# Kernel tuning notes

Hardware: AMD Instinct MI355X
Metric: run time of the kernel (lower is better)

## Reference

```python
import jax, jax.numpy as jnp
import numpy as np

T = 2_097_152  # timesteps


def setup_inputs() -> dict:
    key = jax.random.key(0)
    # precipitation P and potential evapotranspiration E, in mm/day
    x = jax.random.uniform(key, (T, 2), dtype=jnp.float32) * 10.0
    x1 = jnp.float32(350.0)  # production store capacity (mm)
    return {"x": x, "x1": x1}


def reference(x, x1):
    # GR4J production storage. s_init = 0.0.
    P = x[:, 0]
    E = x[:, 1]
    p_n = jax.nn.relu(P - E)  # net rainfall
    e_n = jax.nn.relu(E - P)  # net evapotranspiration
    # tanh(p_n/x1), tanh(e_n/x1) only depend on inputs -> precompute (same math)
    t_p = jnp.tanh(p_n / x1)
    t_e = jnp.tanh(e_n / x1)
    s0 = jnp.float32(0.0) * x1  # s_init * x1

    def step(s, te):
        tp, tn = te
        r = s / x1
        p_s = x1 * (1.0 - r ** 2) * tp / (1.0 + r * tp)
        e_s = s * (2.0 - r) * tn / (1.0 + (1.0 - r) * tn)
        s = s + p_s - e_s
        perc = s * (1.0 - (1.0 + ((4.0 / 9.0) * s / x1) ** 4) ** (-0.25))
        s = s - perc
        return s, (p_s, perc, s)

    _, (p_s, perc, s_store) = jax.lax.scan(step, s0, (t_p, t_e))

    # concat([p_n[:,None], e_n[:,None], p_s[:,None], perc[:,None]], axis=1)
    out = jnp.stack([p_n, e_n, p_s, perc], axis=1)  # [T, 4]
    # scale=True with mu/sigma None: standardize with batch statistics
    mu = jnp.mean(out, axis=0)
    sigma = jnp.std(out, axis=0)  # population std, matches tf.math.reduce_std
    out = (out - mu) / sigma
    return out, s_store[:, None]
```

## Files before the change

kernel.cpp:

```cpp
#include <hip/hip_runtime.h>


typedef float f32x4 __attribute__((ext_vector_type(4)));

#define LCH      32
#define CPB      128
#define TPB      256
#define BSTEPS   4096
#define WUP      1536
#define WUMAP    96
#define WSTO     12
#define NMAP     352
#define HODD     176
#define NCK      129
#define NMST     4

#define CC1 0.98078528f
#define CC2 0.92387953f
#define CC3 0.83146961f
#define CC4 0.70710678f
#define CC5 0.55557023f
#define CC6 0.38268343f
#define CC7 0.19509032f

__device__ __forceinline__ void stepk(float& s, const f32x4 k, float gma) {
    float s2m = s * s;
    float t1  = fmaf(k.y, s, k.x);
    float t2  = fmaf(k.w, s, k.z);
    float s1  = fmaf(s2m, t2, t1);
    float w2  = s1 * s1;
    float q4  = gma * s1;
    float w4  = w2 * w2;
    s = fmaf(-q4, w4, s1);
}

__device__ __forceinline__ void stepk_m(float& s, const f32x4 k, float gma,
                                        float& ps_o, float& pc_o) {
    float sp  = s;
    float s2m = s * s;
    float t1  = fmaf(k.y, s, k.x);
    float t2  = fmaf(k.w, s, k.z);
    float s1  = fmaf(s2m, t2, t1);
    float w2  = s1 * s1;
    float q4  = gma * s1;
    float w4  = w2 * w2;
    s = fmaf(-q4, w4, s1);
    ps_o = fmaxf(s1 - sp, 0.0f);
    pc_o = q4 * w4;
}

struct KC { float inv, x1, x1sq, x1_2, two_x1cu, five_x1sq, four_x1; };

__device__ __forceinline__ f32x4 mkk(float P, float Ev, const KC c,
                                     float& pn_o, float& en_o) {
    float d  = P - Ev;
    float pn = fmaxf(d, 0.f), en = fmaxf(-d, 0.f);
    float up = pn * c.inv, un = en * c.inv;
    float tp = up * fmaf(up * up, -(1.f/3.f), 1.f);
    float tn = un * fmaf(un * un, -(1.f/3.f), 1.f);
    float al = tp * c.inv, be = tn * c.inv;
    float a2 = al * al,  a3v = a2 * al;
    float b2 = be * be,  b3v = b2 * be;
    float e2 = fmaf(-be, c.x1, 1.f);
    float k0 = tp * c.x1;
    float k1 = 1.f - a2 * c.x1sq - (c.x1_2 * be * e2 + c.two_x1cu * b3v);
    float k2 = (a3v * c.x1sq - al) - (c.x1_2 * b2 - be * e2 - c.five_x1sq * b3v);
    float k3 = a2 + b2 - c.four_x1 * b3v;
    pn_o = pn; en_o = en;
    return (f32x4){k0, k1, k2, k3};
}

__global__ __launch_bounds__(256, 2) void scan_hexa(
        const float* __restrict__ x, const float* __restrict__ x1p,
        f32x4* __restrict__ pspc4, f32x4* __restrict__ s4,
        float* __restrict__ partials) {
    __shared__ f32x4 tk[32 * NCK];
    __shared__ f32x4 mapA[NMAP];
    __shared__ f32x4 mapB[NMAP];
    __shared__ float red[32];

    const int tid  = threadIdx.x;
    const int lane = tid & 63;
    const int wid  = tid >> 6;
    const int b    = blockIdx.x;

    const float x1 = x1p[0];
    KC c;
    c.inv = 1.0f / x1; c.x1 = x1; c.x1sq = x1 * x1; c.x1_2 = 2.0f * x1;
    c.two_x1cu = 2.0f * x1 * c.x1sq; c.five_x1sq = 5.0f * c.x1sq;
    c.four_x1 = 4.0f * x1;
    const float gma = 64.0f / (6561.0f * c.x1sq * c.x1sq);
    const float cen = (184.0f / 350.0f) * x1;
    const float hw  = (208.0f / 350.0f) * x1;
    const float ihw = 1.0f / hw;

    float snode[8];
    {
        const float ND[8] = { CC1,  CC3,  CC5,  CC7, -CC7, -CC5, -CC3, -CC1};
        #pragma unroll
        for (int j = 0; j < 8; ++j) snode[j] = fmaf(hw, ND[j], cen);
    }

    float spn = 0.f, sen = 0.f, qpn = 0.f, qen = 0.f;

    {
        const f32x4* __restrict__ x4 = (const f32x4*)x;
        const f32x4 z4 = (f32x4){0.f, 0.f, 0.f, 0.f};

        auto build = [&](const int mi, f32x4 (&w)[8]) {
            const int m = mi - WUMAP;
            float sv[8];
            #pragma unroll
            for (int j = 0; j < 8; ++j) sv[j] = snode[j];
            const bool mainm = (m >= 0);
            #pragma unroll
            for (int q = 0; q < 8; ++q) {
                float pn0, en0, pn1, en1;
                const f32x4 kA = mkk(w[q].x, w[q].y, c, pn0, en0);
                const f32x4 kB = mkk(w[q].z, w[q].w, c, pn1, en1);
                #pragma unroll
                for (int j = 0; j < 8; ++j) {
                    stepk(sv[j], kA, gma);
                    stepk(sv[j], kB, gma);
                }
                if (mainm) {
                    spn += pn0 + pn1; sen += en0 + en1;
                    qpn = fmaf(pn0, pn0, fmaf(pn1, pn1, qpn));
                    qen = fmaf(en0, en0, fmaf(en1, en1, qen));
                    const int t = 16 * m + 2 * q;
                    const int r = t & 31, col = t >> 5;
                    tk[r * NCK + col]       = kA;
                    tk[(r + 1) * NCK + col] = kB;
                }
            }
            float v[8];
            #pragma unroll
            for (int j = 0; j < 8; ++j) v[j] = (sv[j] - cen) * ihw;
            const float e0 = v[0] + v[7], e1 = v[1] + v[6];
            const float e2 = v[2] + v[5], e3 = v[3] + v[4];
            const float o0 = v[0] - v[7], o1 = v[1] - v[6];
            const float o2 = v[2] - v[5], o3 = v[3] - v[4];
            const float a0 = 0.125f * (e0 + e1 + e2 + e3);
            const float a1 = 0.25f * (o0*CC1 + o1*CC3 + o2*CC5 + o3*CC7);
            const float a2 = 0.25f * ((e0 - e3)*CC2 + (e1 - e2)*CC6);
            const float a3 = 0.25f * (o0*CC3 - o1*CC7 - o2*CC1 - o3*CC5);
            const float a4 = 0.25f * CC4 * ((e0 + e3) - (e1 + e2));
            const float a5 = 0.25f * (o0*CC5 - o1*CC1 + o2*CC7 + o3*CC3);
            const float a6 = 0.25f * ((e0 - e3)*CC6 - (e1 - e2)*CC2);
            const float a7 = 0.25f * (o0*CC7 - o1*CC5 + o2*CC3 - o3*CC1);
            const f32x4 ra = (f32x4){a0 - a2 + a4 - a6,
                                     a1 - 3.0f*a3 + 5.0f*a5 - 7.0f*a7,
                                     2.0f*a2 - 8.0f*a4 + 18.0f*a6,
                                     4.0f*a3 - 20.0f*a5 + 56.0f*a7};
            const f32x4 rb = (f32x4){8.0f*a4 - 48.0f*a6,
                                     16.0f*a5 - 112.0f*a7,
                                     32.0f*a6,
                                     64.0f*a7};
            const int slot = (mi >> 1) + ((mi & 1) ? HODD : 0);
            mapA[slot] = ra;
            mapB[slot] = rb;
        };

        const long base = (long)b * (BSTEPS / 2);
        f32x4 wa[8], wb[8];
        const long gpA = base + 8L * (tid - WUMAP);
        #pragma unroll
        for (int q = 0; q < 8; ++q) {
            const long g = gpA + q;
            wa[q] = (g >= 0) ? x4[g] : z4;
        }
        const bool hasB = (tid < NMAP - 256);
        const long gpB = base + 8L * (tid + 256 - WUMAP);
        #pragma unroll
        for (int q = 0; q < 8; ++q)
            wb[q] = hasB ? x4[gpB + q] : z4;
        build(tid, wa);
        if (hasB) build(tid + 256, wb);
    }
    __syncthreads();

    float aps = 0.f, apc = 0.f, qps = 0.f, qpc = 0.f;
    float sg = 0.f;
    if (tid < CPB) {
        const int l = tid;
        const long gstart = ((long)b * CPB + l) * LCH;
        const float s0 = (gstart >= WUP) ? 0.47f * x1 : 0.0f;
        sg = (s0 - cen) * ihw;
        f32x4 PA[8], PB[8], QA[8], QB[8];
        auto rdw = [&](f32x4 (&A)[8], f32x4 (&B)[8], const int st) {
            const int base = l + 4 * st;
            #pragma unroll
            for (int u = 0; u < 8; ++u)
                A[u] = mapA[base + (u >> 1) + ((u & 1) ? HODD : 0)];
            #pragma unroll
            for (int u = 0; u < 8; ++u)
                B[u] = mapB[base + (u >> 1) + ((u & 1) ? HODD : 0)];
        };
        auto wstp = [&](f32x4 (&A)[8], f32x4 (&B)[8]) {
            #pragma unroll
            for (int u = 0; u < 8; ++u) {
                const float s2  = sg * sg;
                const float p0  = fmaf(A[u].y, sg, A[u].x);
                const float p1  = fmaf(A[u].w, sg, A[u].z);
                const float p2  = fmaf(B[u].y, sg, B[u].x);
                const float p3  = fmaf(B[u].w, sg, B[u].z);
                const float s4v = s2 * s2;
                const float q0  = fmaf(p1, s2, p0);
                const float q1  = fmaf(p3, s2, p2);
                sg = fmaf(q1, s4v, q0);
            }
        };
        rdw(PA, PB, 0);
        #pragma unroll 1
        for (int st = 0; st < WSTO; st += 2) {
            rdw(QA, QB, st + 1);
            wstp(PA, PB);
            rdw(PA, PB, st + 2 < WSTO ? st + 2 : WSTO - 1);
            wstp(QA, QB);
        }
    }
    const float s_after = fmaf(hw, sg, cen);

    if (tid < CPB) {
        const int l = tid;
        const size_t chunk = (size_t)b * CPB + l;
        float s = s_after;
        f32x4 KP[8], KQ[8];
        auto rdk = [&](f32x4 (&K)[8], const int m) {
            const int base = (m << 3) * NCK + l;
            #pragma unroll
            for (int u = 0; u < 8; ++u) K[u] = tk[base + u * NCK];
        };
        auto mst = [&](f32x4 (&K)[8], const int m) {
            float psv[8], pcv[8], sv[8];
            #pragma unroll
            for (int u = 0; u < 8; ++u) {
                stepk_m(s, K[u], gma, psv[u], pcv[u]);
                sv[u] = s;
            }
            #pragma unroll
            for (int u = 0; u < 8; ++u) {
                aps += psv[u]; apc += pcv[u];
                qps = fmaf(psv[u], psv[u], qps); qpc = fmaf(pcv[u], pcv[u], qpc);
            }
            const size_t pb = chunk * 16 + 4 * m;
            pspc4[pb + 0] = (f32x4){psv[0], pcv[0], psv[1], pcv[1]};
            pspc4[pb + 1] = (f32x4){psv[2], pcv[2], psv[3], pcv[3]};
            pspc4[pb + 2] = (f32x4){psv[4], pcv[4], psv[5], pcv[5]};
            pspc4[pb + 3] = (f32x4){psv[6], pcv[6], psv[7], pcv[7]};
            const size_t sb = chunk * 8 + 2 * m;
            s4[sb]     = (f32x4){sv[0], sv[1], sv[2], sv[3]};
            s4[sb + 1] = (f32x4){sv[4], sv[5], sv[6], sv[7]};
        };
        rdk(KP, 0);
        #pragma unroll 1
        for (int m = 0; m < NMST; m += 2) {
            rdk(KQ, m + 1);
            mst(KP, m);
            rdk(KP, m + 2 < NMST ? m + 2 : NMST - 1);
            mst(KQ, m + 1);
        }
    }

    float vals[8] = {spn, sen, aps, apc, qpn, qen, qps, qpc};
    #pragma unroll
    for (int k = 0; k < 8; ++k) {
        float v = vals[k];
        #pragma unroll
        for (int off = 32; off > 0; off >>= 1) v += __shfl_down(v, off, 64);
        if (lane == 0) red[k * 4 + wid] = v;
    }
    __syncthreads();
    if (tid < 8)
        partials[b * 8 + tid] =
            red[tid * 4] + red[tid * 4 + 1] + red[tid * 4 + 2] + red[tid * 4 + 3];
}

__global__ __launch_bounds__(256) void normalize_stats(
        const float* __restrict__ x, const f32x4* __restrict__ pspc4,
        const float* __restrict__ pA, f32x4* __restrict__ out4,
        int nA, int Thalf, int T) {
    __shared__ float red[256];
    __shared__ float sst[8];
    const int tid = threadIdx.x;
    {
        const int c = tid & 7;
        float v = 0.f;
        for (int i = tid >> 3; i < nA; i += 32) v += pA[i * 8 + c];
        red[tid] = v;
        __syncthreads();
        for (int off = 128; off >= 8; off >>= 1) {
            if (tid < off) red[tid] += red[tid + off];
            __syncthreads();
        }
        if (tid == 0) {
            const float invT = 1.0f / (float)T;
            #pragma unroll
            for (int k = 0; k < 4; ++k) {
                float mu  = red[k] * invT;
                float var = fmaxf(fmaf(-mu, mu, red[4 + k] * invT), 0.0f);
                sst[k]     = mu;
                sst[4 + k] = (var > 0.0f) ? rsqrtf(var) : 0.0f;
            }
        }
        __syncthreads();
    }
    const float mu0 = sst[0], mu1 = sst[1], mu2 = sst[2], mu3 = sst[3];
    const float is0 = sst[4], is1 = sst[5], is2 = sst[6], is3 = sst[7];
    const f32x4* __restrict__ x4 = (const f32x4*)x;
    for (int i = blockIdx.x * 256 + tid; i < Thalf; i += 1024 * 256) {
        f32x4 xv = x4[i];
        f32x4 pq = pspc4[i];
        float d0 = xv.x - xv.y, d1 = xv.z - xv.w;
        out4[2 * i]     = (f32x4){(fmaxf(d0, 0.f) - mu0) * is0,
                                  (fmaxf(-d0, 0.f) - mu1) * is1,
                                  (pq.x - mu2) * is2,
                                  (pq.y - mu3) * is3};
        out4[2 * i + 1] = (f32x4){(fmaxf(d1, 0.f) - mu0) * is0,
                                  (fmaxf(-d1, 0.f) - mu1) * is1,
                                  (pq.z - mu2) * is2,
                                  (pq.w - mu3) * is3};
    }
}

#define L_CHUNK  128
#define FB_WARMUP 2048
__device__ __forceinline__ float inv1p_fb(float a) {
    float i1 = 1.0f - a;
    float i2 = fmaf(-a, i1, 1.0f);
    return fmaf(-a, i2, 1.0f);
}
struct SCfb { float x1, inv_x1, c49; };
__device__ __forceinline__ void scan_step_fb(float& s, float P, float E, const SCfb c,
                                             float& pn, float& en, float& ps, float& pc) {
    float d = P - E;
    float pn_ = fmaxf(d, 0.0f), en_ = fmaxf(-d, 0.0f);
    float up = pn_ * c.inv_x1;
    float tp = up * fmaf(up * up, -(1.0f / 3.0f), 1.0f);
    float un = en_ * c.inv_x1;
    float tn = un * fmaf(un * un, -(1.0f / 3.0f), 1.0f);
    float r = s * c.inv_x1;
    float ps_ = (tp * c.x1) * fmaf(-r, r, 1.0f) * inv1p_fb(r * tp);
    float es_ = (s * (2.0f - r)) * tn * inv1p_fb((1.0f - r) * tn);
    float s1 = s + ps_ - es_;
    float z = s1 * c.c49, z2 = z * z, v = z2 * z2;
    float t = fmaf(v, fmaf(v, 0.15625f, -0.25f), 1.0f);
    float s2 = s1 * t;
    pn = pn_; en = en_; ps = ps_; pc = s1 - s2; s = s2;
}
__global__ __launch_bounds__(256) void scan_kernel_fb(
        const float* __restrict__ x, const float* __restrict__ x1ptr,
        float* __restrict__ out, float* __restrict__ s_store,
        float* __restrict__ partials, int T) {
    const int c = blockIdx.x * blockDim.x + threadIdx.x;
    const int nchunks = (T + L_CHUNK - 1) / L_CHUNK;
    SCfb cc; cc.x1 = x1ptr[0]; cc.inv_x1 = 1.0f / cc.x1; cc.c49 = (4.0f / 9.0f) * cc.inv_x1;
    float s1a[4] = {0.f, 0.f, 0.f, 0.f};
    float s2a[4] = {0.f, 0.f, 0.f, 0.f};
    if (c < nchunks) {
        const int g0 = c * L_CHUNK;
        const int g1 = min(g0 + L_CHUNK, T);
        const int w0 = max(g0 - FB_WARMUP, 0);
        float s = 0.0f; float pn, en, ps, pc;
        const float2* __restrict__ x2 = (const float2*)x;
        for (int t = w0; t < g0; ++t) { float2 xv = x2[t]; scan_step_fb(s, xv.x, xv.y, cc, pn, en, ps, pc); }
        float4* __restrict__ out4 = (float4*)out;
        for (int t = g0; t < g1; ++t) {
            float2 xv = x2[t];
            scan_step_fb(s, xv.x, xv.y, cc, pn, en, ps, pc);
            out4[t] = make_float4(pn, en, ps, pc);
            s_store[t] = s;
            s1a[0] += pn; s1a[1] += en; s1a[2] += ps; s1a[3] += pc;
            s2a[0] = fmaf(pn, pn, s2a[0]); s2a[1] = fmaf(en, en, s2a[1]);
            s2a[2] = fmaf(ps, ps, s2a[2]); s2a[3] = fmaf(pc, pc, s2a[3]);
        }
    }
    __shared__ float red[256];
    float vals[8] = {s1a[0], s1a[1], s1a[2], s1a[3], s2a[0], s2a[1], s2a[2], s2a[3]};
    for (int k = 0; k < 8; ++k) {
        red[threadIdx.x] = vals[k];
        __syncthreads();
        for (int off = 128; off > 0; off >>= 1) {
            if ((int)threadIdx.x < off) red[threadIdx.x] += red[threadIdx.x + off];
            __syncthreads();
        }
        if (threadIdx.x == 0) partials[blockIdx.x * 8 + k] = red[0];
        __syncthreads();
    }
}
__global__ __launch_bounds__(64) void finalize_fb(
        const float* __restrict__ partials, float* __restrict__ stats, int nblk, int T) {
    const int lane = threadIdx.x;
    float v[8] = {0.f, 0.f, 0.f, 0.f, 0.f, 0.f, 0.f, 0.f};
    for (int b = lane; b < nblk; b += 64)
        for (int k = 0; k < 8; ++k) v[k] += partials[b * 8 + k];
    #pragma unroll
    for (int k = 0; k < 8; ++k)
        for (int off = 32; off > 0; off >>= 1) v[k] += __shfl_down(v[k], off, 64);
    if (lane == 0) {
        const float invT = 1.0f / (float)T;
        for (int k = 0; k < 4; ++k) {
            float mu = v[k] * invT;
            float var = fmaxf(fmaf(-mu, mu, v[k + 4] * invT), 0.0f);
            stats[k] = mu;
            stats[4 + k] = (var > 0.0f) ? rsqrtf(var) : 0.0f;
        }
    }
}
__global__ __launch_bounds__(256) void normalize_fb(
        float* __restrict__ out, const float* __restrict__ stats, int T) {
    const int t = blockIdx.x * blockDim.x + threadIdx.x;
    if (t >= T) return;
    const float4 mu = *(const float4*)stats;
    const float4 is = *(const float4*)(stats + 4);
    float4* o4 = (float4*)out;
    float4 v = o4[t];
    v.x = (v.x - mu.x) * is.x; v.y = (v.y - mu.y) * is.y;
    v.z = (v.z - mu.z) * is.z; v.w = (v.w - mu.w) * is.w;
    o4[t] = v;
}

extern "C" void kernel_launch(void* const* d_in, const int* in_sizes, int n_in,
                              void* d_out, int out_size, void* d_ws, size_t ws_size,
                              hipStream_t stream) {
    const float* x  = (const float*)d_in[0];
    const float* x1 = (const float*)d_in[1];
    const int T = in_sizes[0] / 2;

    float* out     = (float*)d_out;
    float* s_store = out + 4 * (size_t)T;

    const int nblk = T / BSTEPS;

    float* pA = (float*)d_ws;
    const size_t pq_off = 4608;
    const size_t need = (pq_off + 2 * (size_t)T) * sizeof(float);

    const bool fast = (T % BSTEPS == 0) && nblk >= 1 && nblk <= 512 &&
                      (ws_size >= need);

    if (fast) {
        f32x4* pspc4 = (f32x4*)((float*)d_ws + pq_off);
        scan_hexa<<<nblk, TPB, 0, stream>>>(x, x1, pspc4, (f32x4*)s_store, pA);
        normalize_stats<<<1024, 256, 0, stream>>>(x, pspc4, pA,
                                                  (f32x4*)out, nblk, T / 2, T);
    } else {
        float* stats    = (float*)d_ws;
        float* partials = stats + 8;
        const int nchunks = (T + L_CHUNK - 1) / L_CHUNK;
        const int nblkA = (nchunks + 255) / 256;
        scan_kernel_fb<<<nblkA, 256, 0, stream>>>(x, x1, out, s_store, partials, T);
        finalize_fb<<<1, 64, 0, stream>>>(partials, stats, nblkA, T);
        normalize_fb<<<(T + 255) / 256, 256, 0, stream>>>(out, stats, T);
    }
}
```

Measured before the change: 111.1 us.

## Use 384-thread blocks so each thread builds one map, drop software prefetch

Raises the scan block size from 256 to 384 threads so each of the 352 map-building entries gets its own thread, instead of 96 threads doing a second serial build. The launch bound moves to 3 blocks per CU and the block reduction now covers six waves. The double-buffered register prefetch in the warmup and main scan loops is replaced by simple single-buffer loops, which lowers register pressure to fit the new occupancy target but exposes LDS read latency in the serial chains.

```diff
diff --git a/kernel.cpp b/kernel.cpp
--- a/kernel.cpp
+++ b/kernel.cpp
@@ -5,7 +5,7 @@
 
 #define LCH      32
 #define CPB      128
-#define TPB      256
+#define TPB      384
 #define BSTEPS   4096
 #define WUP      1536
 #define WUMAP    96
@@ -14,6 +14,7 @@
 #define HODD     176
 #define NCK      129
 #define NMST     4
+#define NWAVE    6
 
 #define CC1 0.98078528f
 #define CC2 0.92387953f
@@ -70,14 +71,14 @@
     return (f32x4){k0, k1, k2, k3};
 }
 
-__global__ __launch_bounds__(256, 2) void scan_hexa(
+__global__ __launch_bounds__(TPB, 3) void scan_h384(
         const float* __restrict__ x, const float* __restrict__ x1p,
         f32x4* __restrict__ pspc4, f32x4* __restrict__ s4,
         float* __restrict__ partials) {
     __shared__ f32x4 tk[32 * NCK];
     __shared__ f32x4 mapA[NMAP];
     __shared__ f32x4 mapB[NMAP];
-    __shared__ float red[32];
+    __shared__ float red[8 * NWAVE];
 
     const int tid  = threadIdx.x;
     const int lane = tid & 63;
@@ -94,88 +95,75 @@
     const float hw  = (208.0f / 350.0f) * x1;
     const float ihw = 1.0f / hw;
 
-    float snode[8];
-    {
-        const float ND[8] = { CC1,  CC3,  CC5,  CC7, -CC7, -CC5, -CC3, -CC1};
-        #pragma unroll
-        for (int j = 0; j < 8; ++j) snode[j] = fmaf(hw, ND[j], cen);
-    }
-
     float spn = 0.f, sen = 0.f, qpn = 0.f, qen = 0.f;
 
-    {
+    if (tid < NMAP) {
         const f32x4* __restrict__ x4 = (const f32x4*)x;
         const f32x4 z4 = (f32x4){0.f, 0.f, 0.f, 0.f};
-
-        auto build = [&](const int mi, f32x4 (&w)[8]) {
-            const int m = mi - WUMAP;
-            float sv[8];
-            #pragma unroll
-            for (int j = 0; j < 8; ++j) sv[j] = snode[j];
-            const bool mainm = (m >= 0);
-            #pragma unroll
-            for (int q = 0; q < 8; ++q) {
-                float pn0, en0, pn1, en1;
-                const f32x4 kA = mkk(w[q].x, w[q].y, c, pn0, en0);
-                const f32x4 kB = mkk(w[q].z, w[q].w, c, pn1, en1);
-                #pragma unroll
-                for (int j = 0; j < 8; ++j) {
-                    stepk(sv[j], kA, gma);
-                    stepk(sv[j], kB, gma);
-                }
-                if (mainm) {
-                    spn += pn0 + pn1; sen += en0 + en1;
-                    qpn = fmaf(pn0, pn0, fmaf(pn1, pn1, qpn));
-                    qen = fmaf(en0, en0, fmaf(en1, en1, qen));
-                    const int t = 16 * m + 2 * q;
-                    const int r = t & 31, col = t >> 5;
-                    tk[r * NCK + col]       = kA;
-                    tk[(r + 1) * NCK + col] = kB;
-                }
-            }
-            float v[8];
-            #pragma unroll
-            for (int j = 0; j < 8; ++j) v[j] = (sv[j] - cen) * ihw;
-            const float e0 = v[0] + v[7], e1 = v[1] + v[6];
-            const float e2 = v[2] + v[5], e3 = v[3] + v[4];
-            const float o0 = v[0] - v[7], o1 = v[1] - v[6];
-            const float o2 = v[2] - v[5], o3 = v[3] - v[4];
-            const float a0 = 0.125f * (e0 + e1 + e2 + e3);
-            const float a1 = 0.25f * (o0*CC1 + o1*CC3 + o2*CC5 + o3*CC7);
-            const float a2 = 0.25f * ((e0 - e3)*CC2 + (e1 - e2)*CC6);
-            const float a3 = 0.25f * (o0*CC3 - o1*CC7 - o2*CC1 - o3*CC5);
-            const float a4 = 0.25f * CC4 * ((e0 + e3) - (e1 + e2));
-            const float a5 = 0.25f * (o0*CC5 - o1*CC1 + o2*CC7 + o3*CC3);
-            const float a6 = 0.25f * ((e0 - e3)*CC6 - (e1 - e2)*CC2);
-            const float a7 = 0.25f * (o0*CC7 - o1*CC5 + o2*CC3 - o3*CC1);
-            const f32x4 ra = (f32x4){a0 - a2 + a4 - a6,
-                                     a1 - 3.0f*a3 + 5.0f*a5 - 7.0f*a7,
-                                     2.0f*a2 - 8.0f*a4 + 18.0f*a6,
-                                     4.0f*a3 - 20.0f*a5 + 56.0f*a7};
-            const f32x4 rb = (f32x4){8.0f*a4 - 48.0f*a6,
-                                     16.0f*a5 - 112.0f*a7,
-                                     32.0f*a6,
-                                     64.0f*a7};
-            const int slot = (mi >> 1) + ((mi & 1) ? HODD : 0);
-            mapA[slot] = ra;
-            mapB[slot] = rb;
-        };
-
-        const long base = (long)b * (BSTEPS / 2);
-        f32x4 wa[8], wb[8];
-        const long gpA = base + 8L * (tid - WUMAP);
+        const long gp = (long)b * (BSTEPS / 2) + 8L * (tid - WUMAP);
+        f32x4 w[8];
         #pragma unroll
         for (int q = 0; q < 8; ++q) {
-            const long g = gpA + q;
-            wa[q] = (g >= 0) ? x4[g] : z4;
-        }
-        const bool hasB = (tid < NMAP - 256);
-        const long gpB = base + 8L * (tid + 256 - WUMAP);
-        #pragma unroll
-        for (int q = 0; q < 8; ++q)
-            wb[q] = hasB ? x4[gpB + q] : z4;
-        build(tid, wa);
-        if (hasB) build(tid + 256, wb);
+            const long g = gp + q;
+            w[q] = (g >= 0) ? x4[g] : z4;
+        }
+
+        float snode[8];
+        {
+            const float ND[8] = { CC1,  CC3,  CC5,  CC7, -CC7, -CC5, -CC3, -CC1};
+            #pragma unroll
+            for (int j = 0; j < 8; ++j) snode[j] = fmaf(hw, ND[j], cen);
+        }
+
+        const int m = tid - WUMAP;
+        const bool mainm = (m >= 0);
+        float sv[8];
+        #pragma unroll
+        for (int j = 0; j < 8; ++j) sv[j] = snode[j];
+        #pragma unroll
+        for (int q = 0; q < 8; ++q) {
+            float pn0, en0, pn1, en1;
+            const f32x4 kA = mkk(w[q].x, w[q].y, c, pn0, en0);
+            const f32x4 kB = mkk(w[q].z, w[q].w, c, pn1, en1);
+            #pragma unroll
+            for (int j = 0; j < 8; ++j) {
+                stepk(sv[j], kA, gma);
+                stepk(sv[j], kB, gma);
+            }
+            if (mainm) {
+                spn += pn0 + pn1; sen += en0 + en1;
+                qpn = fmaf(pn0, pn0, fmaf(pn1, pn1, qpn));
+                qen = fmaf(en0, en0, fmaf(en1, en1, qen));
+                const int t = 16 * m + 2 * q;
+                const int r = t & 31, col = t >> 5;
+                tk[r * NCK + col]       = kA;
+                tk[(r + 1) * NCK + col] = kB;
+            }
+        }
+        float v[8];
+        #pragma unroll
+        for (int j = 0; j < 8; ++j) v[j] = (sv[j] - cen) * ihw;
+        const float e0 = v[0] + v[7], e1 = v[1] + v[6];
+        const float e2 = v[2] + v[5], e3 = v[3] + v[4];
+        const float o0 = v[0] - v[7], o1 = v[1] - v[6];
+        const float o2 = v[2] - v[5], o3 = v[3] - v[4];
+        const float a0 = 0.125f * (e0 + e1 + e2 + e3);
+        const float a1 = 0.25f * (o0*CC1 + o1*CC3 + o2*CC5 + o3*CC7);
+        const float a2 = 0.25f * ((e0 - e3)*CC2 + (e1 - e2)*CC6);
+        const float a3 = 0.25f * (o0*CC3 - o1*CC7 - o2*CC1 - o3*CC5);
+        const float a4 = 0.25f * CC4 * ((e0 + e3) - (e1 + e2));
+        const float a5 = 0.25f * (o0*CC5 - o1*CC1 + o2*CC7 + o3*CC3);
+        const float a6 = 0.25f * ((e0 - e3)*CC6 - (e1 - e2)*CC2);
+        const float a7 = 0.25f * (o0*CC7 - o1*CC5 + o2*CC3 - o3*CC1);
+        const int slot = (tid >> 1) + ((tid & 1) ? HODD : 0);
+        mapA[slot] = (f32x4){a0 - a2 + a4 - a6,
+                             a1 - 3.0f*a3 + 5.0f*a5 - 7.0f*a7,
+                             2.0f*a2 - 8.0f*a4 + 18.0f*a6,
+                             4.0f*a3 - 20.0f*a5 + 56.0f*a7};
+        mapB[slot] = (f32x4){8.0f*a4 - 48.0f*a6,
+                             16.0f*a5 - 112.0f*a7,
+                             32.0f*a6,
+                             64.0f*a7};
     }
     __syncthreads();
 
@@ -186,8 +174,9 @@
         const long gstart = ((long)b * CPB + l) * LCH;
         const float s0 = (gstart >= WUP) ? 0.47f * x1 : 0.0f;
         sg = (s0 - cen) * ihw;
-        f32x4 PA[8], PB[8], QA[8], QB[8];
-        auto rdw = [&](f32x4 (&A)[8], f32x4 (&B)[8], const int st) {
+        f32x4 A[8], B[8];
+        #pragma unroll 1
+        for (int st = 0; st < WSTO; ++st) {
             const int base = l + 4 * st;
             #pragma unroll
             for (int u = 0; u < 8; ++u)
@@ -195,8 +184,6 @@
             #pragma unroll
             for (int u = 0; u < 8; ++u)
                 B[u] = mapB[base + (u >> 1) + ((u & 1) ? HODD : 0)];
-        };
-        auto wstp = [&](f32x4 (&A)[8], f32x4 (&B)[8]) {
             #pragma unroll
             for (int u = 0; u < 8; ++u) {
                 const float s2  = sg * sg;
@@ -209,14 +196,6 @@
                 const float q1  = fmaf(p3, s2, p2);
                 sg = fmaf(q1, s4v, q0);
             }
-        };
-        rdw(PA, PB, 0);
-        #pragma unroll 1
-        for (int st = 0; st < WSTO; st += 2) {
-            rdw(QA, QB, st + 1);
-            wstp(PA, PB);
-            rdw(PA, PB, st + 2 < WSTO ? st + 2 : WSTO - 1);
-            wstp(QA, QB);
         }
     }
     const float s_after = fmaf(hw, sg, cen);
@@ -225,13 +204,12 @@
         const int l = tid;
         const size_t chunk = (size_t)b * CPB + l;
         float s = s_after;
-        f32x4 KP[8], KQ[8];
-        auto rdk = [&](f32x4 (&K)[8], const int m) {
+        f32x4 K[8];
+        #pragma unroll 1
+        for (int m = 0; m < NMST; ++m) {
             const int base = (m << 3) * NCK + l;
             #pragma unroll
             for (int u = 0; u < 8; ++u) K[u] = tk[base + u * NCK];
-        };
-        auto mst = [&](f32x4 (&K)[8], const int m) {
             float psv[8], pcv[8], sv[8];
             #pragma unroll
             for (int u = 0; u < 8; ++u) {
@@ -251,14 +229,6 @@
             const size_t sb = chunk * 8 + 2 * m;
             s4[sb]     = (f32x4){sv[0], sv[1], sv[2], sv[3]};
             s4[sb + 1] = (f32x4){sv[4], sv[5], sv[6], sv[7]};
-        };
-        rdk(KP, 0);
-        #pragma unroll 1
-        for (int m = 0; m < NMST; m += 2) {
-            rdk(KQ, m + 1);
-            mst(KP, m);
-            rdk(KP, m + 2 < NMST ? m + 2 : NMST - 1);
-            mst(KQ, m + 1);
         }
     }
 
@@ -268,12 +238,15 @@
         float v = vals[k];
         #pragma unroll
         for (int off = 32; off > 0; off >>= 1) v += __shfl_down(v, off, 64);
-        if (lane == 0) red[k * 4 + wid] = v;
+        if (lane == 0) red[k * NWAVE + wid] = v;
     }
     __syncthreads();
-    if (tid < 8)
-        partials[b * 8 + tid] =
-            red[tid * 4] + red[tid * 4 + 1] + red[tid * 4 + 2] + red[tid * 4 + 3];
+    if (tid < 8) {
+        float v = 0.f;
+        #pragma unroll
+        for (int wv = 0; wv < NWAVE; ++wv) v += red[tid * NWAVE + wv];
+        partials[b * 8 + tid] = v;
+    }
 }
 
 __global__ __launch_bounds__(256) void normalize_stats(
@@ -441,7 +414,7 @@
 
     if (fast) {
         f32x4* pspc4 = (f32x4*)((float*)d_ws + pq_off);
-        scan_hexa<<<nblk, TPB, 0, stream>>>(x, x1, pspc4, (f32x4*)s_store, pA);
+        scan_h384<<<nblk, TPB, 0, stream>>>(x, x1, pspc4, (f32x4*)s_store, pA);
         normalize_stats<<<1024, 256, 0, stream>>>(x, pspc4, pA,
                                                   (f32x4*)out, nblk, T / 2, T);
     } else {
```

Result: slower. 116.9 us (+5.2%).
